# Kernel optimization log

Measured on AMD Instinct MI355X. Metric: run time of the kernel, lower is better.

The kernel has to match this reference:

```python
import jax, jax.numpy as jnp
import numpy as np

V = 256       # num_variables
D = 512       # hidden_dim
B = 1024      # batch


def setup_inputs() -> dict:
    key = jax.random.key(0)
    ks = jax.random.split(key, 8)
    s1 = 1.0 / np.sqrt(V + 1)
    s2 = 1.0 / np.sqrt(D)
    return {
        "x": jax.random.normal(ks[0], (B, V), dtype=jnp.float32),
        "adjacency": jax.random.normal(ks[1], (V, V), dtype=jnp.float32),
        "W1": jax.random.normal(ks[2], (V, D, V + 1), dtype=jnp.float32) * s1,
        "b1": jax.random.normal(ks[3], (V, D), dtype=jnp.float32) * s1,
        "W2": jax.random.normal(ks[4], (V, D, D), dtype=jnp.float32) * s2,
        "b2": jax.random.normal(ks[5], (V, D), dtype=jnp.float32) * s2,
        "W3": jax.random.normal(ks[6], (V, D), dtype=jnp.float32) * s2,
        "b3": jax.random.normal(ks[7], (V,), dtype=jnp.float32) * s2,
    }


def reference(x, adjacency, W1, b1, W2, b2, W3, b3):
    # weighted_x[b, i] = (x @ A.T)[b, i]
    wx = x @ adjacency.T  # [B, V]
    # combined input for variable i: cat([x, wx[:, i:i+1]]) -> width V+1
    # build [B, V, V+1] by broadcasting x across the variable axis
    x_b = jnp.broadcast_to(x[:, None, :], (x.shape[0], V, V))
    comb = jnp.concatenate([x_b, wx[:, :, None]], axis=-1)  # [B, V, V+1]
    # per-variable 3-layer MLP, batched over the variable axis i
    h1 = jax.nn.relu(jnp.einsum('bij,idj->bid', comb, W1) + b1)   # [B, V, D]
    h2 = jax.nn.relu(jnp.einsum('bid,ied->bie', h1, W2) + b2)     # [B, V, D]
    out = jnp.einsum('bid,id->bi', h2, W3) + b3                   # [B, V]
    return out
```

## Files before the change

### kernel.cpp

```cpp
#include <hip/hip_runtime.h>
#include <stdint.h>

#define VNUM 256
#define DNUM 512
#define BNUM 1024

typedef __attribute__((ext_vector_type(8))) short bf16x8;
typedef __attribute__((ext_vector_type(4))) float f32x4;

__device__ __forceinline__ uint16_t f2bf(float f) {
    uint32_t u = __float_as_uint(f);
    uint32_t r = (u + 0x7FFFu + ((u >> 16) & 1u)) >> 16;
    return (uint16_t)r;
}

__device__ __forceinline__ void gl_lds16(const void* g, void* l) {
    __builtin_amdgcn_global_load_lds(
        (const __attribute__((address_space(1))) uint32_t*)g,
        (__attribute__((address_space(3))) uint32_t*)l, 16, 0, 0);
}

__device__ __forceinline__ void stage_slice(const uint16_t* __restrict__ gbase,
                                            int kstride, uint16_t* lbase, int l) {
    #pragma unroll
    for (int p = 0; p < 4; p++) {
        const int c = p * 64 + l;
        const int r = c >> 2, k2 = c & 3;
        const int gk2 = k2 ^ ((r >> 1) & 3);
        gl_lds16(gbase + (size_t)r * kstride + gk2 * 8, lbase + p * 512);
    }
}

__global__ __launch_bounds__(256) void wx_kernel(const float* __restrict__ x,
                                                 const float* __restrict__ adj,
                                                 float* __restrict__ wx) {
    __shared__ float xs[64][36];
    __shared__ float as_[64][36];
    const int b0 = blockIdx.x * 64, i0 = blockIdx.y * 64;
    const int t = threadIdx.x;
    const int tx = t & 15, ty = t >> 4;
    const int lr = t >> 2, lk = (t & 3) * 8;
    float c[4][4] = {};
    for (int k0 = 0; k0 < 256; k0 += 32) {
        __syncthreads();
        *(float4*)&xs[lr][lk]      = *(const float4*)&x[(size_t)(b0 + lr) * VNUM + k0 + lk];
        *(float4*)&xs[lr][lk + 4]  = *(const float4*)&x[(size_t)(b0 + lr) * VNUM + k0 + lk + 4];
        *(float4*)&as_[lr][lk]     = *(const float4*)&adj[(size_t)(i0 + lr) * VNUM + k0 + lk];
        *(float4*)&as_[lr][lk + 4] = *(const float4*)&adj[(size_t)(i0 + lr) * VNUM + k0 + lk + 4];
        __syncthreads();
        #pragma unroll
        for (int kk = 0; kk < 32; kk++) {
            float xv[4], av[4];
            #pragma unroll
            for (int a = 0; a < 4; a++) xv[a] = xs[ty + a * 16][kk];
            #pragma unroll
            for (int b = 0; b < 4; b++) av[b] = as_[tx + b * 16][kk];
            #pragma unroll
            for (int a = 0; a < 4; a++)
                #pragma unroll
                for (int b = 0; b < 4; b++) c[a][b] += xv[a] * av[b];
        }
    }
    #pragma unroll
    for (int a = 0; a < 4; a++)
        #pragma unroll
        for (int b = 0; b < 4; b++)
            wx[(size_t)(b0 + ty + a * 16) * VNUM + i0 + tx + b * 16] = c[a][b];
}

__global__ __launch_bounds__(256) void xcvt_kernel(const float* __restrict__ x,
                                                   uint16_t* __restrict__ xbf) {
    const int idx = (blockIdx.x * 256 + threadIdx.x) * 4;
    float4 v = *(const float4*)&x[idx];
    uint32_t p0 = (uint32_t)f2bf(v.x) | ((uint32_t)f2bf(v.y) << 16);
    uint32_t p1 = (uint32_t)f2bf(v.z) | ((uint32_t)f2bf(v.w) << 16);
    *(uint2*)&xbf[idx] = make_uint2(p0, p1);
}

__global__ __launch_bounds__(256) void w1cvt_kernel(const float* __restrict__ W1,
                                                    uint16_t* __restrict__ W1bf,
                                                    float* __restrict__ w1last) {
    const uint32_t i4   = blockIdx.x * 256 + threadIdx.x;
    const uint32_t base = i4 * 4;
    float4 v = *(const float4*)&W1[base];
    float vv[4] = {v.x, v.y, v.z, v.w};
    #pragma unroll
    for (int j = 0; j < 4; j++) {
        uint32_t pos = base + j;
        uint32_t row = pos / 257u;
        uint32_t k   = pos - row * 257u;
        if (k == 256u) w1last[row] = vv[j];
        else           W1bf[(size_t)row * 256 + k] = f2bf(vv[j]);
    }
}

__global__ __launch_bounds__(256) void w2cvt_kernel(const float* __restrict__ W2,
                                                    uint16_t* __restrict__ W2bf) {
    const size_t idx = ((size_t)blockIdx.x * 256 + threadIdx.x) * 4;
    float4 v = *(const float4*)&W2[idx];
    uint32_t p0 = (uint32_t)f2bf(v.x) | ((uint32_t)f2bf(v.y) << 16);
    uint32_t p1 = (uint32_t)f2bf(v.z) | ((uint32_t)f2bf(v.w) << 16);
    *(uint2*)&W2bf[idx] = make_uint2(p0, p1);
}

__global__ __launch_bounds__(512, 2) void fused_kernel(
        const uint16_t* __restrict__ xbf, const float* __restrict__ wx,
        const uint16_t* __restrict__ W1bf, const float* __restrict__ w1last,
        const float* __restrict__ b1, const uint16_t* __restrict__ W2bf,
        const float* __restrict__ b2, const float* __restrict__ W3,
        const float* __restrict__ b3, float* __restrict__ out) {

    __shared__ __align__(16) uint16_t h1s[16 * 64 * 32];
    __shared__ __align__(16) uint16_t Ws[8 * 4096];
    __shared__ float w1ls[DNUM], b1s[DNUM], b2s[DNUM], w3s[DNUM];
    __shared__ float wxs[64];
    __shared__ float red[8][64];

    const int bid = blockIdx.x;
    const int swz = (bid & 7) * 512 + (bid >> 3);
    const int i   = swz >> 4;
    const int b0  = (swz & 15) * 64;

    const int t  = threadIdx.x;
    const int w  = t >> 6, l = t & 63;
    const int lo = l & 15, q = l >> 4;
    const int sA = (lo >> 1) & 3;

    w1ls[t] = w1last[(size_t)i * DNUM + t];
    b1s[t]  = b1[(size_t)i * DNUM + t];
    b2s[t]  = b2[(size_t)i * DNUM + t];
    w3s[t]  = W3[(size_t)i * DNUM + t];
    if (t < 64) wxs[t] = wx[(size_t)(b0 + t) * VNUM + i];

    #pragma unroll
    for (int p = 0; p < 4; p++) {
        const int cb = p * 512 + w * 64;
        const int c  = cb + l;
        const int kt = c >> 8, cc = c & 255;
        const int r = cc >> 2, k2 = cc & 3;
        const int gk2 = k2 ^ ((r >> 1) & 3);
        gl_lds16(xbf + (size_t)(b0 + r) * VNUM + kt * 32 + gk2 * 8, &h1s[cb * 8]);
    }
    __syncthreads();

    uint16_t* myW = &Ws[w * 4096];
    const uint16_t* W1b = W1bf + ((size_t)i * DNUM + w * 64) * 256;
    const uint16_t* W2b = W2bf + ((size_t)i * DNUM + w * 64) * 512;

    f32x4 acc[4][4];
    #pragma unroll
    for (int a = 0; a < 4; a++)
        #pragma unroll
        for (int b = 0; b < 4; b++) { f32x4 z = {0.f, 0.f, 0.f, 0.f}; acc[a][b] = z; }

    stage_slice(W1b, 256, myW, l);
    #pragma unroll
    for (int kt = 0; kt < 8; kt++) {
        const int cur = (kt & 1) * 2048;
        if (kt < 7) stage_slice(W1b + (kt + 1) * 32, 256, myW + (((kt & 1) ^ 1) * 2048), l);
        if (kt < 7) asm volatile("s_waitcnt vmcnt(4)" ::: "memory");
        else        asm volatile("s_waitcnt vmcnt(0)" ::: "memory");
        bf16x8 af[4], bx[4];
        #pragma unroll
        for (int mt = 0; mt < 4; mt++)
            af[mt] = *(const bf16x8*)&myW[cur + (mt * 16 + lo) * 32 + (q ^ sA) * 8];
        #pragma unroll
        for (int nt = 0; nt < 4; nt++)
            bx[nt] = *(const bf16x8*)&h1s[kt * 2048 + (nt * 16 + lo) * 32 + (q ^ sA) * 8];
        __builtin_amdgcn_s_setprio(1);
        #pragma unroll
        for (int mt = 0; mt < 4; mt++)
            #pragma unroll
            for (int nt = 0; nt < 4; nt++)
                acc[mt][nt] = __builtin_amdgcn_mfma_f32_16x16x32_bf16(af[mt], bx[nt], acc[mt][nt], 0, 0, 0);
        __builtin_amdgcn_s_setprio(0);
        __builtin_amdgcn_sched_barrier(0);
    }

    __syncthreads();

    #pragma unroll
    for (int mt = 0; mt < 4; mt++) {
        const int dbase = w * 64 + mt * 16 + q * 4;
        const int ktile = dbase >> 5;
        const int dk    = dbase & 31;
        const int slot  = dk >> 3;
        const int sub   = dk & 7;
        #pragma unroll
        for (int nt = 0; nt < 4; nt++) {
            const int b = nt * 16 + lo;
            const float wxv = wxs[b];
            float v0 = acc[mt][nt][0] + wxv * w1ls[dbase + 0] + b1s[dbase + 0];
            float v1 = acc[mt][nt][1] + wxv * w1ls[dbase + 1] + b1s[dbase + 1];
            float v2 = acc[mt][nt][2] + wxv * w1ls[dbase + 2] + b1s[dbase + 2];
            float v3 = acc[mt][nt][3] + wxv * w1ls[dbase + 3] + b1s[dbase + 3];
            uint32_t lo32 = (uint32_t)f2bf(fmaxf(v0, 0.f)) | ((uint32_t)f2bf(fmaxf(v1, 0.f)) << 16);
            uint32_t hi32 = (uint32_t)f2bf(fmaxf(v2, 0.f)) | ((uint32_t)f2bf(fmaxf(v3, 0.f)) << 16);
            const int sslot = slot ^ sA;
            *(uint2*)&h1s[ktile * 2048 + b * 32 + sslot * 8 + sub] = make_uint2(lo32, hi32);
        }
    }
    #pragma unroll
    for (int a = 0; a < 4; a++)
        #pragma unroll
        for (int b = 0; b < 4; b++) { f32x4 z = {0.f, 0.f, 0.f, 0.f}; acc[a][b] = z; }
    __syncthreads();

    stage_slice(W2b, 512, myW, l);
    #pragma unroll
    for (int kt = 0; kt < 16; kt++) {
        const int cur = (kt & 1) * 2048;
        if (kt < 15) stage_slice(W2b + (kt + 1) * 32, 512, myW + (((kt & 1) ^ 1) * 2048), l);
        if (kt < 15) asm volatile("s_waitcnt vmcnt(4)" ::: "memory");
        else         asm volatile("s_waitcnt vmcnt(0)" ::: "memory");
        bf16x8 ah[4], bw[4];
        #pragma unroll
        for (int mt = 0; mt < 4; mt++)
            ah[mt] = *(const bf16x8*)&h1s[kt * 2048 + (mt * 16 + lo) * 32 + (q ^ sA) * 8];
        #pragma unroll
        for (int nt = 0; nt < 4; nt++)
            bw[nt] = *(const bf16x8*)&myW[cur + (nt * 16 + lo) * 32 + (q ^ sA) * 8];
        __builtin_amdgcn_s_setprio(1);
        #pragma unroll
        for (int mt = 0; mt < 4; mt++)
            #pragma unroll
            for (int nt = 0; nt < 4; nt++)
                acc[mt][nt] = __builtin_amdgcn_mfma_f32_16x16x32_bf16(ah[mt], bw[nt], acc[mt][nt], 0, 0, 0);
        __builtin_amdgcn_s_setprio(0);
        __builtin_amdgcn_sched_barrier(0);
    }

    #pragma unroll
    for (int mt = 0; mt < 4; mt++) {
        #pragma unroll
        for (int reg = 0; reg < 4; reg++) {
            float v = 0.f;
            #pragma unroll
            for (int nt = 0; nt < 4; nt++) {
                const int e = w * 64 + nt * 16 + lo;
                float h = acc[mt][nt][reg] + b2s[e];
                h = fmaxf(h, 0.f);
                v += h * w3s[e];
            }
            v += __shfl_xor(v, 1, 64);
            v += __shfl_xor(v, 2, 64);
            v += __shfl_xor(v, 4, 64);
            v += __shfl_xor(v, 8, 64);
            if (lo == 0) red[w][mt * 16 + q * 4 + reg] = v;
        }
    }
    __syncthreads();
    if (t < 64) {
        float v = b3[i];
        #pragma unroll
        for (int ww = 0; ww < 8; ww++) v += red[ww][t];
        out[(size_t)(b0 + t) * VNUM + i] = v;
    }
}

extern "C" void kernel_launch(void* const* d_in, const int* in_sizes, int n_in,
                              void* d_out, int out_size, void* d_ws, size_t ws_size,
                              hipStream_t stream) {
    const float* x   = (const float*)d_in[0];
    const float* adj = (const float*)d_in[1];
    const float* W1  = (const float*)d_in[2];
    const float* b1  = (const float*)d_in[3];
    const float* W2  = (const float*)d_in[4];
    const float* b2  = (const float*)d_in[5];
    const float* W3  = (const float*)d_in[6];
    const float* b3  = (const float*)d_in[7];
    float* out = (float*)d_out;

    char* ws = (char*)d_ws;
    float*    wx     = (float*)ws;
    uint16_t* xbf    = (uint16_t*)(ws + (1 << 20));
    float*    w1last = (float*)(ws + (1 << 20) + (1 << 19));
    char*     p      = ws + (2 << 20);
    uint16_t* W1bf   = (uint16_t*)p;
    p += (size_t)VNUM * DNUM * 256 * 2;
    uint16_t* W2bf   = (uint16_t*)p;

    wx_kernel<<<dim3(16, 4), 256, 0, stream>>>(x, adj, wx);
    xcvt_kernel<<<256, 256, 0, stream>>>(x, xbf);
    w1cvt_kernel<<<(VNUM * DNUM * 257) / (4 * 256), 256, 0, stream>>>(W1, W1bf, w1last);
    w2cvt_kernel<<<(size_t)(VNUM * DNUM * DNUM) / (4 * 256), 256, 0, stream>>>(W2, W2bf);
    fused_kernel<<<4096, 512, 0, stream>>>(xbf, wx, W1bf, w1last, b1, W2bf, b2, W3, b3, out);
}
```

Before: 837.0 us.

## Load weights directly into registers and convert W2 in-kernel, drop LDS staging

Removes the separate W2 fp32-to-bf16 conversion kernel and its workspace. The fused kernel now reads fp32 W2 straight from global memory into registers and converts it to bf16 on the fly. W1 fragments are also loaded directly into registers with a two-deep software prefetch instead of being staged through LDS. Dropping the weight LDS buffer lets launch bounds ask for 4 blocks per CU, aiming at higher occupancy. The cost is that each of the 16 blocks per variable rereads W2 in fp32, doubling the bytes per reread, with less coalesced per-lane 16-byte loads and extra conversion ALU work inside the hot loop.

```diff
diff --git a/kernel.cpp b/kernel.cpp
--- a/kernel.cpp
+++ b/kernel.cpp
@@ -1,4 +1,5 @@
 #include <hip/hip_runtime.h>
+#include <hip/hip_bf16.h>
 #include <stdint.h>
 
 #define VNUM 256
@@ -20,15 +21,13 @@
         (__attribute__((address_space(3))) uint32_t*)l, 16, 0, 0);
 }
 
-__device__ __forceinline__ void stage_slice(const uint16_t* __restrict__ gbase,
-                                            int kstride, uint16_t* lbase, int l) {
-    #pragma unroll
-    for (int p = 0; p < 4; p++) {
-        const int c = p * 64 + l;
-        const int r = c >> 2, k2 = c & 3;
-        const int gk2 = k2 ^ ((r >> 1) & 3);
-        gl_lds16(gbase + (size_t)r * kstride + gk2 * 8, lbase + p * 512);
-    }
+__device__ __forceinline__ bf16x8 cvt8(float4 f0, float4 f1) {
+    union { __hip_bfloat162 h[4]; bf16x8 v; } u;
+    u.h[0] = __float22bfloat162_rn(make_float2(f0.x, f0.y));
+    u.h[1] = __float22bfloat162_rn(make_float2(f0.z, f0.w));
+    u.h[2] = __float22bfloat162_rn(make_float2(f1.x, f1.y));
+    u.h[3] = __float22bfloat162_rn(make_float2(f1.z, f1.w));
+    return u.v;
 }
 
 __global__ __launch_bounds__(256) void wx_kernel(const float* __restrict__ x,
@@ -94,24 +93,14 @@
     }
 }
 
-__global__ __launch_bounds__(256) void w2cvt_kernel(const float* __restrict__ W2,
-                                                    uint16_t* __restrict__ W2bf) {
-    const size_t idx = ((size_t)blockIdx.x * 256 + threadIdx.x) * 4;
-    float4 v = *(const float4*)&W2[idx];
-    uint32_t p0 = (uint32_t)f2bf(v.x) | ((uint32_t)f2bf(v.y) << 16);
-    uint32_t p1 = (uint32_t)f2bf(v.z) | ((uint32_t)f2bf(v.w) << 16);
-    *(uint2*)&W2bf[idx] = make_uint2(p0, p1);
-}
-
-__global__ __launch_bounds__(512, 2) void fused_kernel(
+__global__ __launch_bounds__(512, 4) void fused_kernel(
         const uint16_t* __restrict__ xbf, const float* __restrict__ wx,
         const uint16_t* __restrict__ W1bf, const float* __restrict__ w1last,
-        const float* __restrict__ b1, const uint16_t* __restrict__ W2bf,
+        const float* __restrict__ b1, const float* __restrict__ W2,
         const float* __restrict__ b2, const float* __restrict__ W3,
         const float* __restrict__ b3, float* __restrict__ out) {
 
     __shared__ __align__(16) uint16_t h1s[16 * 64 * 32];
-    __shared__ __align__(16) uint16_t Ws[8 * 4096];
     __shared__ float w1ls[DNUM], b1s[DNUM], b2s[DNUM], w3s[DNUM];
     __shared__ float wxs[64];
     __shared__ float red[8][64];
@@ -143,38 +132,43 @@
     }
     __syncthreads();
 
-    uint16_t* myW = &Ws[w * 4096];
-    const uint16_t* W1b = W1bf + ((size_t)i * DNUM + w * 64) * 256;
-    const uint16_t* W2b = W2bf + ((size_t)i * DNUM + w * 64) * 512;
-
     f32x4 acc[4][4];
     #pragma unroll
     for (int a = 0; a < 4; a++)
         #pragma unroll
         for (int b = 0; b < 4; b++) { f32x4 z = {0.f, 0.f, 0.f, 0.f}; acc[a][b] = z; }
 
-    stage_slice(W1b, 256, myW, l);
-    #pragma unroll
-    for (int kt = 0; kt < 8; kt++) {
-        const int cur = (kt & 1) * 2048;
-        if (kt < 7) stage_slice(W1b + (kt + 1) * 32, 256, myW + (((kt & 1) ^ 1) * 2048), l);
-        if (kt < 7) asm volatile("s_waitcnt vmcnt(4)" ::: "memory");
-        else        asm volatile("s_waitcnt vmcnt(0)" ::: "memory");
-        bf16x8 af[4], bx[4];
+    {
+        const uint16_t* a_ptr[4];
         #pragma unroll
         for (int mt = 0; mt < 4; mt++)
-            af[mt] = *(const bf16x8*)&myW[cur + (mt * 16 + lo) * 32 + (q ^ sA) * 8];
-        #pragma unroll
-        for (int nt = 0; nt < 4; nt++)
-            bx[nt] = *(const bf16x8*)&h1s[kt * 2048 + (nt * 16 + lo) * 32 + (q ^ sA) * 8];
-        __builtin_amdgcn_s_setprio(1);
-        #pragma unroll
-        for (int mt = 0; mt < 4; mt++)
+            a_ptr[mt] = W1bf + ((size_t)i * DNUM + w * 64 + mt * 16 + lo) * 256 + q * 8;
+
+        bf16x8 Af[2];
+        Af[0] = *(const bf16x8*)(a_ptr[0]);
+        Af[1] = *(const bf16x8*)(a_ptr[1]);
+
+        #pragma unroll
+        for (int kt = 0; kt < 8; kt++) {
+            bf16x8 bx[4];
             #pragma unroll
             for (int nt = 0; nt < 4; nt++)
-                acc[mt][nt] = __builtin_amdgcn_mfma_f32_16x16x32_bf16(af[mt], bx[nt], acc[mt][nt], 0, 0, 0);
-        __builtin_amdgcn_s_setprio(0);
-        __builtin_amdgcn_sched_barrier(0);
+                bx[nt] = *(const bf16x8*)&h1s[kt * 2048 + (nt * 16 + lo) * 32 + (q ^ sA) * 8];
+            #pragma unroll
+            for (int mt = 0; mt < 4; mt++) {
+                const int g = kt * 4 + mt;
+                bf16x8 a = Af[g & 1];
+                if (g + 2 < 32) {
+                    const int gn = g + 2;
+                    Af[g & 1] = *(const bf16x8*)(a_ptr[gn & 3] + (gn >> 2) * 32);
+                }
+                __builtin_amdgcn_s_setprio(1);
+                #pragma unroll
+                for (int nt = 0; nt < 4; nt++)
+                    acc[mt][nt] = __builtin_amdgcn_mfma_f32_16x16x32_bf16(a, bx[nt], acc[mt][nt], 0, 0, 0);
+                __builtin_amdgcn_s_setprio(0);
+            }
+        }
     }
 
     __syncthreads();
@@ -206,28 +200,41 @@
         for (int b = 0; b < 4; b++) { f32x4 z = {0.f, 0.f, 0.f, 0.f}; acc[a][b] = z; }
     __syncthreads();
 
-    stage_slice(W2b, 512, myW, l);
-    #pragma unroll
-    for (int kt = 0; kt < 16; kt++) {
-        const int cur = (kt & 1) * 2048;
-        if (kt < 15) stage_slice(W2b + (kt + 1) * 32, 512, myW + (((kt & 1) ^ 1) * 2048), l);
-        if (kt < 15) asm volatile("s_waitcnt vmcnt(4)" ::: "memory");
-        else         asm volatile("s_waitcnt vmcnt(0)" ::: "memory");
-        bf16x8 ah[4], bw[4];
-        #pragma unroll
-        for (int mt = 0; mt < 4; mt++)
-            ah[mt] = *(const bf16x8*)&h1s[kt * 2048 + (mt * 16 + lo) * 32 + (q ^ sA) * 8];
+    {
+        const float* b_ptr[4];
         #pragma unroll
         for (int nt = 0; nt < 4; nt++)
-            bw[nt] = *(const bf16x8*)&myW[cur + (nt * 16 + lo) * 32 + (q ^ sA) * 8];
-        __builtin_amdgcn_s_setprio(1);
-        #pragma unroll
-        for (int mt = 0; mt < 4; mt++)
-            #pragma unroll
-            for (int nt = 0; nt < 4; nt++)
-                acc[mt][nt] = __builtin_amdgcn_mfma_f32_16x16x32_bf16(ah[mt], bw[nt], acc[mt][nt], 0, 0, 0);
-        __builtin_amdgcn_s_setprio(0);
-        __builtin_amdgcn_sched_barrier(0);
+            b_ptr[nt] = W2 + ((size_t)i * DNUM + w * 64 + nt * 16 + lo) * DNUM + q * 8;
+
+        float4 F[2][2];
+        F[0][0] = *(const float4*)(b_ptr[0]);
+        F[0][1] = *(const float4*)(b_ptr[0] + 4);
+        F[1][0] = *(const float4*)(b_ptr[1]);
+        F[1][1] = *(const float4*)(b_ptr[1] + 4);
+
+        #pragma unroll
+        for (int kt = 0; kt < 16; kt++) {
+            bf16x8 ah[4];
+            #pragma unroll
+            for (int mt = 0; mt < 4; mt++)
+                ah[mt] = *(const bf16x8*)&h1s[kt * 2048 + (mt * 16 + lo) * 32 + (q ^ sA) * 8];
+            #pragma unroll
+            for (int nt = 0; nt < 4; nt++) {
+                const int g = kt * 4 + nt;
+                float4 f0 = F[g & 1][0], f1 = F[g & 1][1];
+                if (g + 2 < 64) {
+                    const int gn = g + 2;
+                    F[g & 1][0] = *(const float4*)(b_ptr[gn & 3] + (gn >> 2) * 32);
+                    F[g & 1][1] = *(const float4*)(b_ptr[gn & 3] + (gn >> 2) * 32 + 4);
+                }
+                bf16x8 bw = cvt8(f0, f1);
+                __builtin_amdgcn_s_setprio(1);
+                #pragma unroll
+                for (int mt = 0; mt < 4; mt++)
+                    acc[mt][nt] = __builtin_amdgcn_mfma_f32_16x16x32_bf16(ah[mt], bw, acc[mt][nt], 0, 0, 0);
+                __builtin_amdgcn_s_setprio(0);
+            }
+        }
     }
 
     #pragma unroll
@@ -275,14 +282,10 @@
     float*    wx     = (float*)ws;
     uint16_t* xbf    = (uint16_t*)(ws + (1 << 20));
     float*    w1last = (float*)(ws + (1 << 20) + (1 << 19));
-    char*     p      = ws + (2 << 20);
-    uint16_t* W1bf   = (uint16_t*)p;
-    p += (size_t)VNUM * DNUM * 256 * 2;
-    uint16_t* W2bf   = (uint16_t*)p;
+    uint16_t* W1bf   = (uint16_t*)(ws + (2 << 20));
 
     wx_kernel<<<dim3(16, 4), 256, 0, stream>>>(x, adj, wx);
     xcvt_kernel<<<256, 256, 0, stream>>>(x, xbf);
     w1cvt_kernel<<<(VNUM * DNUM * 257) / (4 * 256), 256, 0, stream>>>(W1, W1bf, w1last);
-    w2cvt_kernel<<<(size_t)(VNUM * DNUM * DNUM) / (4 * 256), 256, 0, stream>>>(W2, W2bf);
-    fused_kernel<<<4096, 512, 0, stream>>>(xbf, wx, W1bf, w1last, b1, W2bf, b2, W3, b3, out);
-}
+    fused_kernel<<<4096, 512, 0, stream>>>(xbf, wx, W1bf, w1last, b1, W2, b2, W3, b3, out);
+}
```

Result: slower. 1.032 ms (+23.3%).
